# Kernel tuning notes

Measured on AMD Instinct MI355X. Metric: run time of the kernel, lower is better.

## Reference

```python
import jax, jax.numpy as jnp
import numpy as np


def setup_inputs() -> dict:
    key0 = jax.random.key(0)
    kq, kk, kv = jax.random.split(key0, 3)
    B, S, E = 4, 2048, 1024
    query = jax.random.normal(kq, (B, S, E), dtype=jnp.float32)
    key = jax.random.normal(kk, (B, S, E), dtype=jnp.float32)
    value = jax.random.normal(kv, (B, S, E), dtype=jnp.float32)
    attn_mask = jnp.zeros((B, S, S), dtype=jnp.float32)
    return {"query": query, "key": key, "value": value, "attn_mask": attn_mask}


def reference(query, key, value, attn_mask):
    # qk = Q K^T / sqrt(E) + mask; softmax over last dim; dropout is
    # identity in eval mode (reference baseline); out = attn @ V.
    E = query.shape[-1]
    scale = 1.0 / jnp.sqrt(jnp.asarray(E, dtype=query.dtype))
    qk = jnp.einsum("bqe,bke->bqk", query, key) * scale + attn_mask
    attn = jax.nn.softmax(qk, axis=-1)
    out = jnp.einsum("bqk,bke->bqe", attn, value)
    return out
```

## Files before the change

kernel.cpp:

```cpp
#include <hip/hip_runtime.h>
#include <stdint.h>
#include <math.h>

typedef unsigned short u16;
typedef short bf16x8 __attribute__((ext_vector_type(8)));
typedef unsigned short u16x8 __attribute__((ext_vector_type(8)));
typedef unsigned short u16x4 __attribute__((ext_vector_type(4)));
typedef float f32x4 __attribute__((ext_vector_type(4)));

#define LOG2E 1.4426950408889634f

__device__ __forceinline__ float bf2f(u16 u) {
  union { unsigned int i; float f; } v; v.i = ((unsigned int)u) << 16; return v.f;
}
__device__ __forceinline__ u16 f2bf(float f) {
  union { float ff; unsigned int i; } v; v.ff = f;
  unsigned int x = v.i;
  return (u16)((x + 0x7FFFu + ((x >> 16) & 1u)) >> 16);
}

__global__ __launch_bounds__(256)
void cvt_scale(const float* __restrict__ src, u16* __restrict__ dst, long n, float scale)
{
  long i = ((long)blockIdx.x * 256 + threadIdx.x) * 8;
  if (i + 8 > n) return;
  f32x4 a = *(const f32x4*)&src[i];
  f32x4 b = *(const f32x4*)&src[i + 4];
  u16x8 o;
#pragma unroll
  for (int j = 0; j < 4; j++) { o[j] = f2bf(a[j] * scale); o[4 + j] = f2bf(b[j] * scale); }
  *(u16x8*)&dst[i] = o;
}

__global__ __launch_bounds__(256)
void transcvt_v(const float* __restrict__ V, u16* __restrict__ VT, int S, int E)
{
  __shared__ u16 t[64][72];
  const int b = blockIdx.z;
  const float* Vb = V + (long)b * S * E;
  u16* VTb = VT + (long)b * S * E;
  const int k0 = blockIdx.x * 64, n0 = blockIdx.y * 64;
  const int tid = threadIdx.x;
#pragma unroll
  for (int p = 0; p < 2; p++) {
    int kk = p * 32 + (tid >> 3);
    int nn = (tid & 7) * 8;
    f32x4 a = *(const f32x4*)&Vb[(long)(k0 + kk) * E + n0 + nn];
    f32x4 c = *(const f32x4*)&Vb[(long)(k0 + kk) * E + n0 + nn + 4];
#pragma unroll
    for (int j = 0; j < 4; j++) { t[nn + j][kk] = f2bf(a[j]); t[nn + 4 + j][kk] = f2bf(c[j]); }
  }
  __syncthreads();
#pragma unroll
  for (int p = 0; p < 2; p++) {
    int nn = p * 32 + (tid >> 3);
    int kk = (tid & 7) * 8;
    u16x8 u;
#pragma unroll
    for (int j = 0; j < 8; j++) u[j] = t[nn][kk + j];
    *(u16x8*)&VTb[(long)(n0 + nn) * S + k0 + kk] = u;
  }
}

template<int COUT>
__global__ __launch_bounds__(256, 3)
void gemm_bf16(const u16* __restrict__ A, int lda, long aRowOff,
               const u16* __restrict__ B, int ldb, long bBatchStride,
               void* __restrict__ Cp, int ldc, long cRowOff,
               int K, long g0, int S)
{
  const int tid  = threadIdx.x;
  const int lane = tid & 63;
  const int wave = tid >> 6;
  const long gTile = g0 + (long)blockIdx.y * 128;
  const int  b     = (int)(gTile / S);
  const int  nTile = blockIdx.x * 128;

  __shared__ u16 As[8192];
  __shared__ u16 Bs[8192];

  const u16* aG = A + (gTile - aRowOff) * (long)lda;
  const u16* bG = B + (long)b * bBatchStride;

  const int r0 = wave * 32 + (lane & 15);
  const int c0 = (lane >> 4) * 8;
  const u16* ag = aG + (long)r0 * lda + c0;
  const u16* bg = bG + (long)(nTile + r0) * ldb + c0;
  u16* asw = As + wave * 2048 + lane * 8;
  u16* bsw = Bs + wave * 2048 + lane * 8;

  f32x4 acc[4][4];
#pragma unroll
  for (int i = 0; i < 4; i++)
#pragma unroll
    for (int j = 0; j < 4; j++) acc[i][j] = (f32x4){0.f, 0.f, 0.f, 0.f};

  const int qmi = (wave >> 1) * 4;
  const int qni = (wave & 1) * 4;

  for (int k0 = 0; k0 < K; k0 += 64) {
    u16x8 a00 = *(const u16x8*)&ag[k0];
    u16x8 a01 = *(const u16x8*)&ag[k0 + 32];
    u16x8 a10 = *(const u16x8*)&ag[(long)16 * lda + k0];
    u16x8 a11 = *(const u16x8*)&ag[(long)16 * lda + k0 + 32];
    u16x8 b00 = *(const u16x8*)&bg[k0];
    u16x8 b01 = *(const u16x8*)&bg[k0 + 32];
    u16x8 b10 = *(const u16x8*)&bg[(long)16 * ldb + k0];
    u16x8 b11 = *(const u16x8*)&bg[(long)16 * ldb + k0 + 32];
    *(u16x8*)&asw[0]    = a00;
    *(u16x8*)&asw[512]  = a01;
    *(u16x8*)&asw[1024] = a10;
    *(u16x8*)&asw[1536] = a11;
    *(u16x8*)&bsw[0]    = b00;
    *(u16x8*)&bsw[512]  = b01;
    *(u16x8*)&bsw[1024] = b10;
    *(u16x8*)&bsw[1536] = b11;
    __syncthreads();

#pragma unroll
    for (int ks = 0; ks < 2; ks++) {
      bf16x8 af[4], bfr[4];
#pragma unroll
      for (int rt = 0; rt < 4; rt++)
        af[rt] = *(const bf16x8*)&As[(qmi + rt) * 1024 + ks * 512 + lane * 8];
#pragma unroll
      for (int ct = 0; ct < 4; ct++)
        bfr[ct] = *(const bf16x8*)&Bs[(qni + ct) * 1024 + ks * 512 + lane * 8];
#pragma unroll
      for (int rt = 0; rt < 4; rt++)
#pragma unroll
        for (int ct = 0; ct < 4; ct++)
          acc[rt][ct] = __builtin_amdgcn_mfma_f32_16x16x32_bf16(af[rt], bfr[ct], acc[rt][ct], 0, 0, 0);
    }
    __syncthreads();
  }

  const int qm = (wave >> 1) * 64;
  const int qn = (wave & 1) * 64;
  const int lm16 = lane & 15;
  const int lr = (lane >> 4) * 4;
#pragma unroll
  for (int rt = 0; rt < 4; rt++) {
#pragma unroll
    for (int ct = 0; ct < 4; ct++) {
      long gr = gTile + qm + rt * 16 + lr;
      int  cc = nTile + qn + ct * 16 + lm16;
#pragma unroll
      for (int i = 0; i < 4; i++) {
        if (COUT == 0)
          ((u16*)Cp)[(gr + i - cRowOff) * (long)ldc + cc] = f2bf(acc[rt][ct][i]);
        else
          ((float*)Cp)[(gr + i - cRowOff) * (long)ldc + cc] = acc[rt][ct][i];
      }
    }
  }
}

template<int BMODE, int HASMASK, int COUT>
__global__ __launch_bounds__(256, 2)
void gemm_slow(const void* __restrict__ Ap, int lda, long aRowOff,
               const void* __restrict__ Bp, int ldb, long bBatchStride,
               void* __restrict__ Cp, int ldc, long cRowOff,
               const float* __restrict__ maskf,
               int K, float scale, long g0, int S)
{
  const int tid  = threadIdx.x;
  const int lane = tid & 63;
  const int wave = tid >> 6;
  const long gTile = g0 + (long)blockIdx.y * 128;
  const int  b     = (int)(gTile / S);
  const int  nTile = blockIdx.x * 128;

  __shared__ u16 As[128][40];
  __shared__ u16 Bs[128][40];

  const int qm = (wave >> 1) * 64;
  const int qn = (wave & 1) * 64;

  f32x4 acc[4][4];
#pragma unroll
  for (int i = 0; i < 4; i++)
#pragma unroll
    for (int j = 0; j < 4; j++) acc[i][j] = (f32x4){0.f, 0.f, 0.f, 0.f};

  const float* Af = (const float*)Ap + (gTile - aRowOff) * (long)lda;
  const u16*   Ab16 = (const u16*)Ap + (gTile - aRowOff) * (long)lda;
  const float* Bf = (const float*)Bp + (long)b * bBatchStride;

  const int lm = lane & 15;
  const int lk = (lane >> 4) * 8;

  for (int k0 = 0; k0 < K; k0 += 32) {
    if (BMODE == 1) {
      int srow = tid >> 2, scol = (tid & 3) * 8;
#pragma unroll
      for (int p = 0; p < 2; p++) {
        int r = p * 64 + srow;
        *(u16x8*)&As[r][scol] = *(const u16x8*)&Ab16[(long)r * lda + k0 + scol];
      }
    } else {
      int srow = tid >> 3, scol = (tid & 7) * 4;
#pragma unroll
      for (int p = 0; p < 4; p++) {
        int r = p * 32 + srow;
        f32x4 a = *(const f32x4*)&Af[(long)r * lda + k0 + scol];
        u16x4 o;
#pragma unroll
        for (int j = 0; j < 4; j++) o[j] = f2bf(a[j]);
        *(u16x4*)&As[r][scol] = o;
      }
    }
    if (BMODE == 0) {
      int srow = tid >> 3, scol = (tid & 7) * 4;
#pragma unroll
      for (int p = 0; p < 4; p++) {
        int r = p * 32 + srow;
        f32x4 a = *(const f32x4*)&Bf[(long)(nTile + r) * ldb + k0 + scol];
        u16x4 o;
#pragma unroll
        for (int j = 0; j < 4; j++) o[j] = f2bf(a[j]);
        *(u16x4*)&Bs[r][scol] = o;
      }
    }
    __syncthreads();

    bf16x8 af[4], bfr[4];
#pragma unroll
    for (int rt = 0; rt < 4; rt++)
      af[rt] = *(const bf16x8*)&As[qm + rt * 16 + lm][lk];
    if (BMODE == 0) {
#pragma unroll
      for (int ct = 0; ct < 4; ct++)
        bfr[ct] = *(const bf16x8*)&Bs[qn + ct * 16 + lm][lk];
    } else {
#pragma unroll
      for (int ct = 0; ct < 4; ct++) {
        const float* vp = Bf + (long)(k0 + lk) * ldb + nTile + qn + ct * 16 + lm;
#pragma unroll
        for (int j = 0; j < 8; j++) bfr[ct][j] = (short)f2bf(vp[(long)j * ldb]);
      }
    }
#pragma unroll
    for (int rt = 0; rt < 4; rt++)
#pragma unroll
      for (int ct = 0; ct < 4; ct++)
        acc[rt][ct] = __builtin_amdgcn_mfma_f32_16x16x32_bf16(af[rt], bfr[ct], acc[rt][ct], 0, 0, 0);
    __syncthreads();
  }

  const int lr = (lane >> 4) * 4;
#pragma unroll
  for (int rt = 0; rt < 4; rt++) {
#pragma unroll
    for (int ct = 0; ct < 4; ct++) {
      long gr = gTile + qm + rt * 16 + lr;
      int  cc = nTile + qn + ct * 16 + lm;
#pragma unroll
      for (int i = 0; i < 4; i++) {
        float v = acc[rt][ct][i] * scale;
        if (HASMASK) v += maskf[(gr + i) * (long)ldc + cc];
        if (COUT == 0)
          ((u16*)Cp)[(gr + i - cRowOff) * (long)ldc + cc] = f2bf(v);
        else
          ((float*)Cp)[(gr + i - cRowOff) * (long)ldc + cc] = v;
      }
    }
  }
}

template<int HASMASK>
__global__ __launch_bounds__(256)
void softmax_rows(u16* __restrict__ Sbuf, const float* __restrict__ mask,
                  long g0, int ncols)
{
  const long row = blockIdx.x;
  u16* rp = Sbuf + row * (long)ncols;
  const int tid = threadIdx.x;

  u16x8 u = *(const u16x8*)&rp[tid * 8];
  float x[8];
  if (HASMASK) {
    const float* mp = mask + (g0 + row) * (long)ncols + tid * 8;
    f32x4 m0 = *(const f32x4*)&mp[0];
    f32x4 m1 = *(const f32x4*)&mp[4];
#pragma unroll
    for (int i = 0; i < 4; i++) { x[i] = bf2f(u[i]) + m0[i]; x[4 + i] = bf2f(u[4 + i]) + m1[i]; }
  } else {
#pragma unroll
    for (int i = 0; i < 8; i++) x[i] = bf2f(u[i]);
  }
  float m = -3.0e38f;
#pragma unroll
  for (int i = 0; i < 8; i++) m = fmaxf(m, x[i]);
#pragma unroll
  for (int off = 32; off; off >>= 1) m = fmaxf(m, __shfl_xor(m, off, 64));
  __shared__ float redm[4];
  if ((tid & 63) == 0) redm[tid >> 6] = m;
  __syncthreads();
  m = fmaxf(fmaxf(redm[0], redm[1]), fmaxf(redm[2], redm[3]));

  float e[8];
  float s = 0.f;
#pragma unroll
  for (int i = 0; i < 8; i++) { e[i] = exp2f((x[i] - m) * LOG2E); s += e[i]; }
#pragma unroll
  for (int off = 32; off; off >>= 1) s += __shfl_xor(s, off, 64);
  __shared__ float reds[4];
  if ((tid & 63) == 0) reds[tid >> 6] = s;
  __syncthreads();
  s = reds[0] + reds[1] + reds[2] + reds[3];

  float inv = 1.0f / s;
  u16x8 o;
#pragma unroll
  for (int i = 0; i < 8; i++) o[i] = f2bf(e[i] * inv);
  *(u16x8*)&rp[tid * 8] = o;
}

extern "C" void kernel_launch(void* const* d_in, const int* in_sizes, int n_in,
                              void* d_out, int out_size, void* d_ws, size_t ws_size,
                              hipStream_t stream)
{
  const float* Q    = (const float*)d_in[0];
  const float* Km   = (const float*)d_in[1];
  const float* V    = (const float*)d_in[2];
  const float* mask = (const float*)d_in[3];
  float* out = (float*)d_out;

  const long qsz = in_sizes[0];
  const long msz = in_sizes[3];
  const long E = 1024;
  const long S = (msz / qsz) * E;
  const long B = qsz / (S * E);
  const long G = B * S;
  const float scale = 1.0f / sqrtf((float)E);

  const size_t convBytes = (size_t)(3 * qsz) * 2;
  const size_t rowBytes  = (size_t)S * 2;
  char* w = (char*)d_ws;
  size_t avail = ws_size;
  const bool haveConv = (ws_size >= convBytes + 128 * rowBytes);

  u16 *Qb = nullptr, *Kb = nullptr, *VTb = nullptr;
  if (haveConv) {
    Qb  = (u16*)w;  w += (size_t)qsz * 2;
    Kb  = (u16*)w;  w += (size_t)qsz * 2;
    VTb = (u16*)w;  w += (size_t)qsz * 2;
    avail -= convBytes;
  }
  long Rmax = (long)((avail / rowBytes) / 128) * 128;
  if (Rmax > G) Rmax = G;
  if (Rmax < 128) Rmax = 128;
  u16* Sbuf = (u16*)w;

  if (haveConv) {
    cvt_scale<<<dim3((unsigned)(qsz / 2048)), 256, 0, stream>>>(Q, Qb, qsz, scale);
    cvt_scale<<<dim3((unsigned)(qsz / 2048)), 256, 0, stream>>>(Km, Kb, qsz, 1.0f);
    transcvt_v<<<dim3(S / 64, E / 64, B), 256, 0, stream>>>(V, VTb, (int)S, (int)E);
  }

  for (long g0 = 0; g0 < G; g0 += Rmax) {
    const long R = (G - g0 < Rmax) ? (G - g0) : Rmax;
    if (haveConv) {
      gemm_bf16<0><<<dim3(S / 128, R / 128), 256, 0, stream>>>(
          Qb, (int)E, 0L, Kb, (int)E, S * E,
          Sbuf, (int)S, g0, (int)E, g0, (int)S);
      softmax_rows<1><<<dim3(R), 256, 0, stream>>>(Sbuf, mask, g0, (int)S);
      gemm_bf16<1><<<dim3(E / 128, R / 128), 256, 0, stream>>>(
          Sbuf, (int)S, g0, VTb, (int)S, E * S,
          out, (int)E, 0L, (int)S, g0, (int)S);
    } else {
      gemm_slow<0, 1, 0><<<dim3(S / 128, R / 128), 256, 0, stream>>>(
          Q, (int)E, 0L, Km, (int)E, S * E,
          Sbuf, (int)S, g0, mask, (int)E, scale, g0, (int)S);
      softmax_rows<0><<<dim3(R), 256, 0, stream>>>(Sbuf, nullptr, g0, (int)S);
      gemm_slow<1, 0, 1><<<dim3(E / 128, R / 128), 256, 0, stream>>>(
          Sbuf, (int)S, g0, V, (int)E, S * E,
          out, (int)E, 0L, nullptr, (int)S, 1.0f, g0, (int)S);
    }
  }
}
```

Measured before the change: 319.4 us.

## Enlarge GEMM tiles to 256x128 with 512 threads and grouped block swizzle

Replaces the bf16 GEMM with a 512-thread kernel computing 256x128 tiles, so each B tile loaded into shared memory is reused across twice as many rows. A block-index remap groups blocks into bands of eight rows to improve L2 locality. The kernel can also convert fp32 A/B to bf16 on the fly, so when the workspace cannot hold converted Q/K the separate conversion passes are skipped and the QK strip can be larger. The trade-off is more shared memory and registers per block, which may lower occupancy.

New measurement: 321.9 us. About the same (+0.8%).

```diff
diff --git a/kernel.cpp b/kernel.cpp
--- a/kernel.cpp
+++ b/kernel.cpp
@@ -62,32 +62,45 @@
   }
 }
 
-template<int COUT>
-__global__ __launch_bounds__(256, 3)
-void gemm_bf16(const u16* __restrict__ A, int lda, long aRowOff,
-               const u16* __restrict__ B, int ldb, long bBatchStride,
+template<int AF32, int BF32, int COUT>
+__global__ __launch_bounds__(512, 4)
+void gemm_fast(const void* __restrict__ A_, int lda, long aRowOff,
+               const void* __restrict__ B_, int ldb, long bBatchStride,
                void* __restrict__ Cp, int ldc, long cRowOff,
-               int K, long g0, int S)
-{
+               int K, float aScale, long g0, int S)
+{
+  int gx = gridDim.x, gy = gridDim.y;
+  int bx = blockIdx.x, by = blockIdx.y;
+  if ((gy & 7) == 0) {
+    int f = by * gx + bx;
+    int band = gy >> 3;
+    int u = f & 7, v = f >> 3;
+    by = u * band + (v % band);
+    bx = v / band;
+  }
   const int tid  = threadIdx.x;
   const int lane = tid & 63;
   const int wave = tid >> 6;
-  const long gTile = g0 + (long)blockIdx.y * 128;
+  const long gTile = g0 + (long)by * 256;
   const int  b     = (int)(gTile / S);
-  const int  nTile = blockIdx.x * 128;
-
-  __shared__ u16 As[8192];
+  const int  nTile = bx * 128;
+
+  __shared__ u16 As[16384];
   __shared__ u16 Bs[8192];
 
-  const u16* aG = A + (gTile - aRowOff) * (long)lda;
-  const u16* bG = B + (long)b * bBatchStride;
-
-  const int r0 = wave * 32 + (lane & 15);
-  const int c0 = (lane >> 4) * 8;
-  const u16* ag = aG + (long)r0 * lda + c0;
-  const u16* bg = bG + (long)(nTile + r0) * ldb + c0;
-  u16* asw = As + wave * 2048 + lane * 8;
-  u16* bsw = Bs + wave * 2048 + lane * 8;
+  const float* Af = (const float*)A_ + (gTile - aRowOff) * (long)lda;
+  const u16*   Ab = (const u16*)A_   + (gTile - aRowOff) * (long)lda;
+  const float* Bf = (const float*)B_ + (long)b * bBatchStride;
+  const u16*   Bb = (const u16*)B_   + (long)b * bBatchStride;
+
+  const int l15 = lane & 15;
+  const int lc  = (lane >> 4) * 8;
+
+  const long ar0 = (long)(wave * 32 + l15) * lda + lc;
+  const long ar1 = ar0 + (long)16 * lda;
+  const long br0 = (long)(nTile + wave * 16 + l15) * ldb + lc;
+  u16* as0 = As + wave * 2048 + lane * 8;
+  u16* bs0 = Bs + wave * 1024 + lane * 8;
 
   f32x4 acc[4][4];
 #pragma unroll
@@ -95,26 +108,54 @@
 #pragma unroll
     for (int j = 0; j < 4; j++) acc[i][j] = (f32x4){0.f, 0.f, 0.f, 0.f};
 
-  const int qmi = (wave >> 1) * 4;
-  const int qni = (wave & 1) * 4;
+  const int wm4 = (wave >> 1) * 4;
+  const int wn4 = (wave & 1) * 4;
 
   for (int k0 = 0; k0 < K; k0 += 64) {
-    u16x8 a00 = *(const u16x8*)&ag[k0];
-    u16x8 a01 = *(const u16x8*)&ag[k0 + 32];
-    u16x8 a10 = *(const u16x8*)&ag[(long)16 * lda + k0];
-    u16x8 a11 = *(const u16x8*)&ag[(long)16 * lda + k0 + 32];
-    u16x8 b00 = *(const u16x8*)&bg[k0];
-    u16x8 b01 = *(const u16x8*)&bg[k0 + 32];
-    u16x8 b10 = *(const u16x8*)&bg[(long)16 * ldb + k0];
-    u16x8 b11 = *(const u16x8*)&bg[(long)16 * ldb + k0 + 32];
-    *(u16x8*)&asw[0]    = a00;
-    *(u16x8*)&asw[512]  = a01;
-    *(u16x8*)&asw[1024] = a10;
-    *(u16x8*)&asw[1536] = a11;
-    *(u16x8*)&bsw[0]    = b00;
-    *(u16x8*)&bsw[512]  = b01;
-    *(u16x8*)&bsw[1024] = b10;
-    *(u16x8*)&bsw[1536] = b11;
+    if (AF32) {
+      f32x4 x0 = *(const f32x4*)&Af[ar0 + k0],      x1 = *(const f32x4*)&Af[ar0 + k0 + 4];
+      f32x4 x2 = *(const f32x4*)&Af[ar0 + k0 + 32], x3 = *(const f32x4*)&Af[ar0 + k0 + 36];
+      f32x4 x4 = *(const f32x4*)&Af[ar1 + k0],      x5 = *(const f32x4*)&Af[ar1 + k0 + 4];
+      f32x4 x6 = *(const f32x4*)&Af[ar1 + k0 + 32], x7 = *(const f32x4*)&Af[ar1 + k0 + 36];
+      u16x8 w0, w1, w2, w3;
+#pragma unroll
+      for (int j = 0; j < 4; j++) {
+        w0[j] = f2bf(x0[j] * aScale); w0[4 + j] = f2bf(x1[j] * aScale);
+        w1[j] = f2bf(x2[j] * aScale); w1[4 + j] = f2bf(x3[j] * aScale);
+        w2[j] = f2bf(x4[j] * aScale); w2[4 + j] = f2bf(x5[j] * aScale);
+        w3[j] = f2bf(x6[j] * aScale); w3[4 + j] = f2bf(x7[j] * aScale);
+      }
+      *(u16x8*)&as0[0]    = w0;
+      *(u16x8*)&as0[512]  = w1;
+      *(u16x8*)&as0[1024] = w2;
+      *(u16x8*)&as0[1536] = w3;
+    } else {
+      u16x8 a0 = *(const u16x8*)&Ab[ar0 + k0];
+      u16x8 a1 = *(const u16x8*)&Ab[ar0 + k0 + 32];
+      u16x8 a2 = *(const u16x8*)&Ab[ar1 + k0];
+      u16x8 a3 = *(const u16x8*)&Ab[ar1 + k0 + 32];
+      *(u16x8*)&as0[0]    = a0;
+      *(u16x8*)&as0[512]  = a1;
+      *(u16x8*)&as0[1024] = a2;
+      *(u16x8*)&as0[1536] = a3;
+    }
+    if (BF32) {
+      f32x4 y0 = *(const f32x4*)&Bf[br0 + k0],      y1 = *(const f32x4*)&Bf[br0 + k0 + 4];
+      f32x4 y2 = *(const f32x4*)&Bf[br0 + k0 + 32], y3 = *(const f32x4*)&Bf[br0 + k0 + 36];
+      u16x8 w0, w1;
+#pragma unroll
+      for (int j = 0; j < 4; j++) {
+        w0[j] = f2bf(y0[j]); w0[4 + j] = f2bf(y1[j]);
+        w1[j] = f2bf(y2[j]); w1[4 + j] = f2bf(y3[j]);
+      }
+      *(u16x8*)&bs0[0]   = w0;
+      *(u16x8*)&bs0[512] = w1;
+    } else {
+      u16x8 b0 = *(const u16x8*)&Bb[br0 + k0];
+      u16x8 b1 = *(const u16x8*)&Bb[br0 + k0 + 32];
+      *(u16x8*)&bs0[0]   = b0;
+      *(u16x8*)&bs0[512] = b1;
+    }
     __syncthreads();
 
 #pragma unroll
@@ -122,10 +163,10 @@
       bf16x8 af[4], bfr[4];
 #pragma unroll
       for (int rt = 0; rt < 4; rt++)
-        af[rt] = *(const bf16x8*)&As[(qmi + rt) * 1024 + ks * 512 + lane * 8];
+        af[rt] = *(const bf16x8*)&As[(wm4 + rt) * 1024 + ks * 512 + lane * 8];
 #pragma unroll
       for (int ct = 0; ct < 4; ct++)
-        bfr[ct] = *(const bf16x8*)&Bs[(qni + ct) * 1024 + ks * 512 + lane * 8];
+        bfr[ct] = *(const bf16x8*)&Bs[(wn4 + ct) * 1024 + ks * 512 + lane * 8];
 #pragma unroll
       for (int rt = 0; rt < 4; rt++)
 #pragma unroll
@@ -137,14 +178,13 @@
 
   const int qm = (wave >> 1) * 64;
   const int qn = (wave & 1) * 64;
-  const int lm16 = lane & 15;
   const int lr = (lane >> 4) * 4;
 #pragma unroll
   for (int rt = 0; rt < 4; rt++) {
 #pragma unroll
     for (int ct = 0; ct < 4; ct++) {
       long gr = gTile + qm + rt * 16 + lr;
-      int  cc = nTile + qn + ct * 16 + lm16;
+      int  cc = nTile + qn + ct * 16 + l15;
 #pragma unroll
       for (int i = 0; i < 4; i++) {
         if (COUT == 0)
@@ -335,48 +375,60 @@
   const long G = B * S;
   const float scale = 1.0f / sqrtf((float)E);
 
-  const size_t convBytes = (size_t)(3 * qsz) * 2;
-  const size_t rowBytes  = (size_t)S * 2;
+  const size_t vtB    = (size_t)qsz * 2;
+  const size_t sbFull = (size_t)G * S * 2;
+  const size_t strip1 = (size_t)256 * S * 2;
+
   char* w = (char*)d_ws;
   size_t avail = ws_size;
-  const bool haveConv = (ws_size >= convBytes + 128 * rowBytes);
-
-  u16 *Qb = nullptr, *Kb = nullptr, *VTb = nullptr;
-  if (haveConv) {
-    Qb  = (u16*)w;  w += (size_t)qsz * 2;
-    Kb  = (u16*)w;  w += (size_t)qsz * 2;
-    VTb = (u16*)w;  w += (size_t)qsz * 2;
-    avail -= convBytes;
-  }
-  long Rmax = (long)((avail / rowBytes) / 128) * 128;
+  u16 *VTb = nullptr, *Qb = nullptr, *Kb = nullptr;
+  const bool haveVT = (avail >= vtB + strip1);
+  if (haveVT) { VTb = (u16*)w; w += vtB; avail -= vtB; }
+  const bool haveQK = haveVT && (avail >= 2 * vtB + sbFull);
+  if (haveQK) { Qb = (u16*)w; w += vtB; Kb = (u16*)w; w += vtB; avail -= 2 * vtB; }
+
+  if (haveVT) {
+    long Rmax = (long)((avail / ((size_t)S * 2)) / 256) * 256;
+    if (Rmax > G) Rmax = G;
+    u16* Sbuf = (u16*)w;
+    if (Rmax >= 256) {
+      if (haveQK) {
+        cvt_scale<<<dim3((unsigned)(qsz / 2048)), 256, 0, stream>>>(Q, Qb, qsz, scale);
+        cvt_scale<<<dim3((unsigned)(qsz / 2048)), 256, 0, stream>>>(Km, Kb, qsz, 1.0f);
+      }
+      transcvt_v<<<dim3(S / 64, E / 64, B), 256, 0, stream>>>(V, VTb, (int)S, (int)E);
+
+      for (long g0 = 0; g0 < G; g0 += Rmax) {
+        const long R = (G - g0 < Rmax) ? (G - g0) : Rmax;
+        if (haveQK)
+          gemm_fast<0, 0, 0><<<dim3(S / 128, R / 256), 512, 0, stream>>>(
+              Qb, (int)E, 0L, Kb, (int)E, S * E,
+              Sbuf, (int)S, g0, (int)E, 1.0f, g0, (int)S);
+        else
+          gemm_fast<1, 1, 0><<<dim3(S / 128, R / 256), 512, 0, stream>>>(
+              Q, (int)E, 0L, Km, (int)E, S * E,
+              Sbuf, (int)S, g0, (int)E, scale, g0, (int)S);
+        softmax_rows<1><<<dim3(R), 256, 0, stream>>>(Sbuf, mask, g0, (int)S);
+        gemm_fast<0, 0, 1><<<dim3(E / 128, R / 256), 512, 0, stream>>>(
+            Sbuf, (int)S, g0, VTb, (int)S, E * S,
+            out, (int)E, 0L, (int)S, 1.0f, g0, (int)S);
+      }
+      return;
+    }
+  }
+
+  u16* Sbuf = (u16*)d_ws;
+  long Rmax = (long)((ws_size / ((size_t)S * 2)) / 128) * 128;
   if (Rmax > G) Rmax = G;
   if (Rmax < 128) Rmax = 128;
-  u16* Sbuf = (u16*)w;
-
-  if (haveConv) {
-    cvt_scale<<<dim3((unsigned)(qsz / 2048)), 256, 0, stream>>>(Q, Qb, qsz, scale);
-    cvt_scale<<<dim3((unsigned)(qsz / 2048)), 256, 0, stream>>>(Km, Kb, qsz, 1.0f);
-    transcvt_v<<<dim3(S / 64, E / 64, B), 256, 0, stream>>>(V, VTb, (int)S, (int)E);
-  }
-
   for (long g0 = 0; g0 < G; g0 += Rmax) {
     const long R = (G - g0 < Rmax) ? (G - g0) : Rmax;
-    if (haveConv) {
-      gemm_bf16<0><<<dim3(S / 128, R / 128), 256, 0, stream>>>(
-          Qb, (int)E, 0L, Kb, (int)E, S * E,
-          Sbuf, (int)S, g0, (int)E, g0, (int)S);
-      softmax_rows<1><<<dim3(R), 256, 0, stream>>>(Sbuf, mask, g0, (int)S);
-      gemm_bf16<1><<<dim3(E / 128, R / 128), 256, 0, stream>>>(
-          Sbuf, (int)S, g0, VTb, (int)S, E * S,
-          out, (int)E, 0L, (int)S, g0, (int)S);
-    } else {
-      gemm_slow<0, 1, 0><<<dim3(S / 128, R / 128), 256, 0, stream>>>(
-          Q, (int)E, 0L, Km, (int)E, S * E,
-          Sbuf, (int)S, g0, mask, (int)E, scale, g0, (int)S);
-      softmax_rows<0><<<dim3(R), 256, 0, stream>>>(Sbuf, nullptr, g0, (int)S);
-      gemm_slow<1, 0, 1><<<dim3(E / 128, R / 128), 256, 0, stream>>>(
-          Sbuf, (int)S, g0, V, (int)E, S * E,
-          out, (int)E, 0L, nullptr, (int)S, 1.0f, g0, (int)S);
-    }
-  }
-}
+    gemm_slow<0, 1, 0><<<dim3(S / 128, R / 128), 256, 0, stream>>>(
+        Q, (int)E, 0L, Km, (int)E, S * E,
+        Sbuf, (int)S, g0, mask, (int)E, scale, g0, (int)S);
+    softmax_rows<0><<<dim3(R), 256, 0, stream>>>(Sbuf, nullptr, g0, (int)S);
+    gemm_slow<1, 0, 1><<<dim3(E / 128, R / 128), 256, 0, stream>>>(
+        Sbuf, (int)S, g0, V, (int)E, S * E,
+        out, (int)E, 0L, nullptr, (int)S, 1.0f, g0, (int)S);
+  }
+}
```
